# Optimization experiments

Measured on AMD Instinct MI355X. Metric: run time of the kernel, lower is better.

The kernel has to match this reference:

```python
import jax, jax.numpy as jnp
import numpy as np

B, T, C, HD = 8, 2048, 1024, 64  # batch, seq, feature_size, head_dim = C // n_head


def setup_inputs() -> dict:
    key = jax.random.key(0)
    kx, kq, kk, kv = jax.random.split(key, 4)
    return {
        "x": jax.random.normal(kx, (B, T, C), dtype=jnp.float32),
        "Wq": jax.random.normal(kq, (C, HD), dtype=jnp.float32) * 0.02,
        "Wk": jax.random.normal(kk, (C, HD), dtype=jnp.float32) * 0.02,
        "Wv": jax.random.normal(kv, (C, HD), dtype=jnp.float32) * 0.02,
    }


def reference(x, Wq, Wk, Wv):
    # x: [B, T, C]; W*: [C, HD] (Linear(feature_size, feature_size//n_head, bias=False))
    Bsz, Tlen, Cdim = x.shape
    q = x @ Wq  # [B, T, HD]
    k = x @ Wk
    v = x @ Wv
    scores = jnp.einsum("btd,bsd->bts", q, k)  # [B, T, T]
    causal = jnp.tril(jnp.ones((Tlen, Tlen), dtype=bool))
    # faithful to source: masked_fill(-inf) THEN divide by sqrt(C) (full feature size)
    scores = jnp.where(causal, scores, -jnp.inf) / jnp.sqrt(jnp.float32(Cdim))
    att = jax.nn.softmax(scores, axis=-1)  # dropout p=0.0 (eval) -> identity
    return att @ v  # [B, T, HD]
```

## Files before the change

kernel.cpp:

```cpp
#include <hip/hip_runtime.h>


#define BATCH 8
#define SEQ   2048
#define CIN   1024
#define HDIM  64
#define NROW  (BATCH * SEQ)
#define NQT   (NROW / 16)

typedef __attribute__((ext_vector_type(8))) short bf16x8;
typedef __attribute__((ext_vector_type(4))) short u16x4;
typedef __attribute__((ext_vector_type(4))) float f32x4;

__device__ __forceinline__ unsigned short f2bf(float f) {
  unsigned int u = __builtin_bit_cast(unsigned int, f);
  u += 0x7fffu + ((u >> 16) & 1u);
  return (unsigned short)(u >> 16);
}
__device__ __forceinline__ float bf2f(unsigned short h) {
  return __builtin_bit_cast(float, (unsigned int)h << 16);
}
__device__ __forceinline__ u16x4 pack4(f32x4 a) {
  u16x4 r;
  r[0] = (short)f2bf(a[0]); r[1] = (short)f2bf(a[1]);
  r[2] = (short)f2bf(a[2]); r[3] = (short)f2bf(a[3]);
  return r;
}

__global__ __launch_bounds__(256) void wtrans_k(const float* __restrict__ wq,
                                                const float* __restrict__ wk,
                                                const float* __restrict__ wv,
                                                unsigned short* __restrict__ wt) {
  __shared__ unsigned short lds[64][65];
  const int m  = blockIdx.x >> 4;
  const int c0 = (blockIdx.x & 15) * 64;
  const float* w = (m == 0) ? wq : (m == 1) ? wk : wv;
  const int nl = threadIdx.x & 63, gr = threadIdx.x >> 6;
#pragma unroll
  for (int i = 0; i < 16; ++i) {
    int cl = gr * 16 + i;
    lds[cl][nl] = f2bf(w[(size_t)(c0 + cl) * HDIM + nl]);
  }
  __syncthreads();
#pragma unroll
  for (int i = 0; i < 16; ++i) {
    int n = gr * 16 + i;
    wt[(size_t)m * 65536 + n * CIN + c0 + nl] = lds[nl][n];
  }
}

__global__ __launch_bounds__(512) void qkv_proj_k(const float* __restrict__ x,
                                                  const unsigned short* __restrict__ wt,
                                                  unsigned short* __restrict__ q,
                                                  unsigned short* __restrict__ k,
                                                  unsigned short* __restrict__ vt) {
  __shared__ __align__(16) unsigned char ldsb[28672];
  const int tid  = threadIdx.x;
  const int lane = tid & 63;
  const int w    = tid >> 6;
  const int lr   = lane & 15, lg = lane >> 4;
  const int wm   = w & 1, wn = w >> 1;
  const int row0 = blockIdx.x * 32;

  const int trow  = tid >> 4;
  const int tcol4 = (tid & 15) * 4;
  const float* xg = x + (size_t)(row0 + trow) * CIN + tcol4;
  const int xoff  = trow * 128 + (((tcol4 >> 3) ^ (trow & 7)) << 4) + ((tcol4 & 4) << 1);

  const int wrow_ = tid >> 3;
  const int wg8   = tid & 7;
  const unsigned short* wg[3];
  int woff[3];
#pragma unroll
  for (int c = 0; c < 3; ++c) {
    int wrow = c * 64 + wrow_;
    wg[c]   = wt + (size_t)wrow * CIN + wg8 * 8;
    woff[c] = 4096 + wrow * 128 + ((wg8 ^ (wrow & 7)) << 4);
  }

  f32x4 acc[3];
#pragma unroll
  for (int i = 0; i < 3; ++i) acc[i] = (f32x4){0.f, 0.f, 0.f, 0.f};

  const int arow_off = (wm * 16 + lr) * 128;
  const int brow0    = wn * 48 + lr;

#pragma unroll 1
  for (int t = 0; t < 16; ++t) {
    const int k0 = t * 64;
    f32x4 xv = *(const f32x4*)(xg + k0);
    bf16x8 w0 = *(const bf16x8*)(wg[0] + k0);
    bf16x8 w1 = *(const bf16x8*)(wg[1] + k0);
    bf16x8 w2 = *(const bf16x8*)(wg[2] + k0);
    __syncthreads();
    *(u16x4*)(void*)(ldsb + xoff)    = pack4(xv);
    *(bf16x8*)(void*)(ldsb + woff[0]) = w0;
    *(bf16x8*)(void*)(ldsb + woff[1]) = w1;
    *(bf16x8*)(void*)(ldsb + woff[2]) = w2;
    __syncthreads();
#pragma unroll
    for (int kk = 0; kk < 2; ++kk) {
      const int swz = (((kk << 2) | lg) ^ (lr & 7)) << 4;
      bf16x8 af = *(const bf16x8*)(void*)(ldsb + arow_off + swz);
#pragma unroll
      for (int f = 0; f < 3; ++f) {
        bf16x8 bf_ = *(const bf16x8*)(void*)(ldsb + 4096 + (brow0 + f * 16) * 128 + swz);
        acc[f] = __builtin_amdgcn_mfma_f32_16x16x32_bf16(af, bf_, acc[f], 0, 0, 0);
      }
    }
  }

#pragma unroll
  for (int f = 0; f < 3; ++f) {
    const int gc  = wn * 48 + f * 16;
    const int mat = gc >> 6;
    const int hd  = (gc & 63) + lr;
#pragma unroll
    for (int j = 0; j < 4; ++j) {
      int grow = row0 + wm * 16 + lg * 4 + j;
      float v = acc[f][j];
      if (mat == 0) {
        q[(size_t)grow * HDIM + hd] = f2bf(v * 0.03125f);
      } else if (mat == 1) {
        k[(size_t)grow * HDIM + hd] = f2bf(v);
      } else {
        int b = grow >> 11, tp = grow & 2047;
        vt[((size_t)b * HDIM + hd) * SEQ + tp] = f2bf(v);
      }
    }
  }
}

__global__ __launch_bounds__(64) void attn_k(const unsigned short* __restrict__ q,
                                             const unsigned short* __restrict__ k,
                                             const unsigned short* __restrict__ vt,
                                             float* __restrict__ opart,
                                             float* __restrict__ m_l,
                                             int S) {
  __shared__ __align__(16) unsigned short plds[16][72];
  const int lane = threadIdx.x;
  const int lr = lane & 15, lg = lane >> 4;
  const int blk  = blockIdx.x;
  const int b    = blk & 7;
  const int rest = blk >> 3;
  const int s    = rest % S;
  const int qt   = 127 - rest / S;
  const int row0 = qt * 16;
  const int p    = (b * 128 + qt) * S + s;

  const unsigned short* qb_ = q  + (size_t)b * SEQ * HDIM;
  const unsigned short* kb_ = k  + (size_t)b * SEQ * HDIM;
  const unsigned short* vb_ = vt + (size_t)b * HDIM * SEQ;

  bf16x8 qf0 = *(const bf16x8*)(qb_ + (row0 + lr) * HDIM + lg * 8);
  bf16x8 qf1 = *(const bf16x8*)(qb_ + (row0 + lr) * HDIM + 32 + lg * 8);

  f32x4 o[4];
#pragma unroll
  for (int n = 0; n < 4; ++n) o[n] = (f32x4){0.f, 0.f, 0.f, 0.f};
  float m_run = -INFINITY, l_run = 0.f;
  const int   qrow = row0 + lr;
  const float LOG2E = 1.44269504f;
  const int nt = (row0 + 79) >> 6;
  const int lo = (nt * s) / S;
  const int hi = (nt * (s + 1)) / S;

  for (int t = lo; t < hi; ++t) {
    const int kv = t * 64;
    f32x4 sv[4];
#pragma unroll
    for (int f = 0; f < 4; ++f) sv[f] = (f32x4){0.f, 0.f, 0.f, 0.f};
#pragma unroll
    for (int f = 0; f < 4; ++f) {
      bf16x8 ka0 = *(const bf16x8*)(kb_ + (kv + f * 16 + lr) * HDIM + lg * 8);
      bf16x8 ka1 = *(const bf16x8*)(kb_ + (kv + f * 16 + lr) * HDIM + 32 + lg * 8);
      sv[f] = __builtin_amdgcn_mfma_f32_16x16x32_bf16(ka0, qf0, sv[f], 0, 0, 0);
      sv[f] = __builtin_amdgcn_mfma_f32_16x16x32_bf16(ka1, qf1, sv[f], 0, 0, 0);
    }
    if (kv + 63 > row0) {
#pragma unroll
      for (int f = 0; f < 4; ++f)
#pragma unroll
        for (int j = 0; j < 4; ++j)
          if (kv + f * 16 + lg * 4 + j > qrow) sv[f][j] = -INFINITY;
    }
    float tm = -INFINITY;
#pragma unroll
    for (int f = 0; f < 4; ++f)
#pragma unroll
      for (int j = 0; j < 4; ++j) tm = fmaxf(tm, sv[f][j]);
    tm = fmaxf(tm, __shfl_xor(tm, 16, 64));
    tm = fmaxf(tm, __shfl_xor(tm, 32, 64));
    float m_new = fmaxf(m_run, tm);
    float alpha = (m_run == -INFINITY) ? 0.f : exp2f((m_run - m_new) * LOG2E);
    float mc    = (m_new == -INFINITY) ? 0.f : m_new * LOG2E;
    float ps = 0.f;
#pragma unroll
    for (int f = 0; f < 4; ++f) {
      float p0 = exp2f(sv[f][0] * LOG2E - mc);
      float p1 = exp2f(sv[f][1] * LOG2E - mc);
      float p2 = exp2f(sv[f][2] * LOG2E - mc);
      float p3 = exp2f(sv[f][3] * LOG2E - mc);
      unsigned short r0 = f2bf(p0), r1 = f2bf(p1), r2 = f2bf(p2), r3 = f2bf(p3);
      *(unsigned int*)(&plds[lr][f * 16 + lg * 4])     = (unsigned int)r0 | ((unsigned int)r1 << 16);
      *(unsigned int*)(&plds[lr][f * 16 + lg * 4 + 2]) = (unsigned int)r2 | ((unsigned int)r3 << 16);
      ps += bf2f(r0) + bf2f(r1) + bf2f(r2) + bf2f(r3);
    }
    ps += __shfl_xor(ps, 16, 64);
    ps += __shfl_xor(ps, 32, 64);
    l_run = l_run * alpha + ps;
    m_run = m_new;
#pragma unroll
    for (int j = 0; j < 4; ++j) {
      float aj = __shfl(alpha, lg * 4 + j, 64);
      o[0][j] *= aj; o[1][j] *= aj; o[2][j] *= aj; o[3][j] *= aj;
    }
    __syncthreads();
#pragma unroll
    for (int kk = 0; kk < 2; ++kk) {
      bf16x8 pf = *(const bf16x8*)(&plds[lr][kk * 32 + lg * 8]);
#pragma unroll
      for (int n = 0; n < 4; ++n) {
        bf16x8 vf = *(const bf16x8*)(vb_ + (n * 16 + lr) * SEQ + kv + kk * 32 + lg * 8);
        o[n] = __builtin_amdgcn_mfma_f32_16x16x32_bf16(pf, vf, o[n], 0, 0, 0);
      }
    }
    __syncthreads();
  }

  if (lane < 16) {
    m_l[p * 32 + lane]      = m_run;
    m_l[p * 32 + 16 + lane] = l_run;
  }
#pragma unroll
  for (int j = 0; j < 4; ++j) {
    int r = lg * 4 + j;
#pragma unroll
    for (int n = 0; n < 4; ++n)
      opart[(size_t)p * 1024 + r * 64 + n * 16 + lr] = o[n][j];
  }
}

__global__ __launch_bounds__(256) void combine_k(const float* __restrict__ opart,
                                                 const float* __restrict__ m_l,
                                                 float* __restrict__ out, int S) {
  const float LOG2E = 1.44269504f;
  int idx = blockIdx.x * 256 + threadIdx.x;
  int col = idx & 63;
  int row = idx >> 6;
  int b = row >> 11, t = row & 2047;
  int qt = t >> 4, r = t & 15;
  int pb = (b * 128 + qt) * S;
  float M = -INFINITY;
  for (int s = 0; s < S; ++s) M = fmaxf(M, m_l[(pb + s) * 32 + r]);
  float l = 0.f, o = 0.f;
  for (int s = 0; s < S; ++s) {
    float ms = m_l[(pb + s) * 32 + r];
    float w  = exp2f((ms - M) * LOG2E);
    l += m_l[(pb + s) * 32 + 16 + r] * w;
    o += opart[(size_t)(pb + s) * 1024 + r * 64 + col] * w;
  }
  out[(size_t)row * HDIM + col] = o / l;
}

extern "C" void kernel_launch(void* const* d_in, const int* in_sizes, int n_in,
                              void* d_out, int out_size, void* d_ws, size_t ws_size,
                              hipStream_t stream) {
  const float* x  = (const float*)d_in[0];
  const float* wq = (const float*)d_in[1];
  const float* wk = (const float*)d_in[2];
  const float* wv = (const float*)d_in[3];
  float* outp = (float*)d_out;

  const size_t bf_bytes = ((size_t)3 * NROW * HDIM + 3 * 65536) * 2;
  int S = 4;
  while (S > 1 && (size_t)NQT * S * (32 + 1024) * 4 + bf_bytes > ws_size) S >>= 1;

  float* m_l   = (float*)d_ws;
  float* opart = m_l + (size_t)NQT * S * 32;
  unsigned short* qbuf = (unsigned short*)(opart + (size_t)NQT * S * 1024);
  unsigned short* kbuf = qbuf + (size_t)NROW * HDIM;
  unsigned short* vbuf = kbuf + (size_t)NROW * HDIM;
  unsigned short* wt   = vbuf + (size_t)NROW * HDIM;

  hipLaunchKernelGGL(wtrans_k, dim3(48), dim3(256), 0, stream, wq, wk, wv, wt);
  hipLaunchKernelGGL(qkv_proj_k, dim3(NROW / 32), dim3(512), 0, stream, x, wt, qbuf, kbuf, vbuf);
  hipLaunchKernelGGL(attn_k, dim3(NQT * S), dim3(64), 0, stream, qbuf, kbuf, vbuf, opart, m_l, S);
  hipLaunchKernelGGL(combine_k, dim3(NROW * HDIM / 256), dim3(256), 0, stream, opart, m_l, outp, S);
}
```

Before: 162.6 us.

## Pack four attention waves per block, prefetch K/V tiles, drop block barriers

The attention kernel now runs four independent 64-lane work units per 256-thread block, each with its own shared-memory P buffer. Block-wide __syncthreads are replaced by an LDS waitcnt plus a scheduling barrier. The next K tile is prefetched into registers while the current one is processed, and V fragments are loaded before the softmax so their latency overlaps the exp work. The row sum now uses the fp32 probabilities instead of the bf16-rounded ones. These changes raise register pressure and may lower occupancy.

```diff
diff --git a/kernel.cpp b/kernel.cpp
--- a/kernel.cpp
+++ b/kernel.cpp
@@ -131,22 +131,24 @@
   }
 }
 
-__global__ __launch_bounds__(64) void attn_k(const unsigned short* __restrict__ q,
-                                             const unsigned short* __restrict__ k,
-                                             const unsigned short* __restrict__ vt,
-                                             float* __restrict__ opart,
-                                             float* __restrict__ m_l,
-                                             int S) {
-  __shared__ __align__(16) unsigned short plds[16][72];
-  const int lane = threadIdx.x;
+__global__ __launch_bounds__(256) void attn_k(const unsigned short* __restrict__ q,
+                                              const unsigned short* __restrict__ k,
+                                              const unsigned short* __restrict__ vt,
+                                              float* __restrict__ opart,
+                                              float* __restrict__ m_l,
+                                              int S) {
+  __shared__ __align__(16) unsigned short plds[4][16][72];
+  const int lane = threadIdx.x & 63;
+  const int w    = threadIdx.x >> 6;
   const int lr = lane & 15, lg = lane >> 4;
-  const int blk  = blockIdx.x;
-  const int b    = blk & 7;
-  const int rest = blk >> 3;
+  const int u    = blockIdx.x * 4 + w;
+  const int b    = u & 7;
+  const int rest = u >> 3;
   const int s    = rest % S;
   const int qt   = 127 - rest / S;
   const int row0 = qt * 16;
   const int p    = (b * 128 + qt) * S + s;
+  unsigned short (*pw)[72] = plds[w];
 
   const unsigned short* qb_ = q  + (size_t)b * SEQ * HDIM;
   const unsigned short* kb_ = k  + (size_t)b * SEQ * HDIM;
@@ -165,18 +167,36 @@
   const int lo = (nt * s) / S;
   const int hi = (nt * (s + 1)) / S;
 
+  auto LDK = [&](int kv, bf16x8* dst) {
+#pragma unroll
+    for (int f = 0; f < 4; ++f) {
+      dst[2 * f]     = *(const bf16x8*)(kb_ + (kv + f * 16 + lr) * HDIM + lg * 8);
+      dst[2 * f + 1] = *(const bf16x8*)(kb_ + (kv + f * 16 + lr) * HDIM + 32 + lg * 8);
+    }
+  };
+
+  bf16x8 ka[8];
+  if (lo < hi) LDK(lo * 64, ka);
+
   for (int t = lo; t < hi; ++t) {
     const int kv = t * 64;
     f32x4 sv[4];
 #pragma unroll
-    for (int f = 0; f < 4; ++f) sv[f] = (f32x4){0.f, 0.f, 0.f, 0.f};
-#pragma unroll
     for (int f = 0; f < 4; ++f) {
-      bf16x8 ka0 = *(const bf16x8*)(kb_ + (kv + f * 16 + lr) * HDIM + lg * 8);
-      bf16x8 ka1 = *(const bf16x8*)(kb_ + (kv + f * 16 + lr) * HDIM + 32 + lg * 8);
-      sv[f] = __builtin_amdgcn_mfma_f32_16x16x32_bf16(ka0, qf0, sv[f], 0, 0, 0);
-      sv[f] = __builtin_amdgcn_mfma_f32_16x16x32_bf16(ka1, qf1, sv[f], 0, 0, 0);
-    }
+      sv[f] = (f32x4){0.f, 0.f, 0.f, 0.f};
+      sv[f] = __builtin_amdgcn_mfma_f32_16x16x32_bf16(ka[2 * f],     qf0, sv[f], 0, 0, 0);
+      sv[f] = __builtin_amdgcn_mfma_f32_16x16x32_bf16(ka[2 * f + 1], qf1, sv[f], 0, 0, 0);
+    }
+    bf16x8 kn[8];
+    const bool more = (t + 1 < hi);
+    if (more) LDK(kv + 64, kn);
+    bf16x8 vf[8];
+#pragma unroll
+    for (int kk = 0; kk < 2; ++kk)
+#pragma unroll
+      for (int n = 0; n < 4; ++n)
+        vf[kk * 4 + n] = *(const bf16x8*)(vb_ + (n * 16 + lr) * SEQ + kv + kk * 32 + lg * 8);
+
     if (kv + 63 > row0) {
 #pragma unroll
       for (int f = 0; f < 4; ++f)
@@ -201,10 +221,11 @@
       float p1 = exp2f(sv[f][1] * LOG2E - mc);
       float p2 = exp2f(sv[f][2] * LOG2E - mc);
       float p3 = exp2f(sv[f][3] * LOG2E - mc);
-      unsigned short r0 = f2bf(p0), r1 = f2bf(p1), r2 = f2bf(p2), r3 = f2bf(p3);
-      *(unsigned int*)(&plds[lr][f * 16 + lg * 4])     = (unsigned int)r0 | ((unsigned int)r1 << 16);
-      *(unsigned int*)(&plds[lr][f * 16 + lg * 4 + 2]) = (unsigned int)r2 | ((unsigned int)r3 << 16);
-      ps += bf2f(r0) + bf2f(r1) + bf2f(r2) + bf2f(r3);
+      ps += (p0 + p1) + (p2 + p3);
+      unsigned int lo32 = (unsigned int)f2bf(p0) | ((unsigned int)f2bf(p1) << 16);
+      unsigned int hi32 = (unsigned int)f2bf(p2) | ((unsigned int)f2bf(p3) << 16);
+      uint2 pk; pk.x = lo32; pk.y = hi32;
+      *(uint2*)(&pw[lr][f * 16 + lg * 4]) = pk;
     }
     ps += __shfl_xor(ps, 16, 64);
     ps += __shfl_xor(ps, 32, 64);
@@ -215,17 +236,19 @@
       float aj = __shfl(alpha, lg * 4 + j, 64);
       o[0][j] *= aj; o[1][j] *= aj; o[2][j] *= aj; o[3][j] *= aj;
     }
-    __syncthreads();
+    asm volatile("s_waitcnt lgkmcnt(0)" ::: "memory");
+    __builtin_amdgcn_sched_barrier(0);
 #pragma unroll
     for (int kk = 0; kk < 2; ++kk) {
-      bf16x8 pf = *(const bf16x8*)(&plds[lr][kk * 32 + lg * 8]);
-#pragma unroll
-      for (int n = 0; n < 4; ++n) {
-        bf16x8 vf = *(const bf16x8*)(vb_ + (n * 16 + lr) * SEQ + kv + kk * 32 + lg * 8);
-        o[n] = __builtin_amdgcn_mfma_f32_16x16x32_bf16(pf, vf, o[n], 0, 0, 0);
-      }
-    }
-    __syncthreads();
+      bf16x8 pf = *(const bf16x8*)(&pw[lr][kk * 32 + lg * 8]);
+#pragma unroll
+      for (int n = 0; n < 4; ++n)
+        o[n] = __builtin_amdgcn_mfma_f32_16x16x32_bf16(pf, vf[kk * 4 + n], o[n], 0, 0, 0);
+    }
+    if (more) {
+#pragma unroll
+      for (int f = 0; f < 8; ++f) ka[f] = kn[f];
+    }
   }
 
   if (lane < 16) {
@@ -285,6 +308,6 @@
 
   hipLaunchKernelGGL(wtrans_k, dim3(48), dim3(256), 0, stream, wq, wk, wv, wt);
   hipLaunchKernelGGL(qkv_proj_k, dim3(NROW / 32), dim3(512), 0, stream, x, wt, qbuf, kbuf, vbuf);
-  hipLaunchKernelGGL(attn_k, dim3(NQT * S), dim3(64), 0, stream, qbuf, kbuf, vbuf, opart, m_l, S);
+  hipLaunchKernelGGL(attn_k, dim3(NQT * S / 4), dim3(256), 0, stream, qbuf, kbuf, vbuf, opart, m_l, S);
   hipLaunchKernelGGL(combine_k, dim3(NROW * HDIM / 256), dim3(256), 0, stream, opart, m_l, outp, S);
 }
```

After: 162.2 us. Within noise of the previous version (-0.3%).

## Balance causal attention with split count growing by query tile, pack four waves per block

Applied to the files above, without the earlier changes.

Replaces the fixed per-tile KV split with a variable split count that grows with query-tile index (S = qt/16 + 1), so each work unit covers a roughly equal number of KV tiles. Four independent wavefronts now share one 256-thread block, each with its own LDS slice, and the block-wide barriers become an LDS waitcnt plus a sched barrier. Row sums now come from the fp32 probabilities rather than the bf16-rounded ones, and the combine kernel decodes the new unit layout. It aims to remove tail imbalance and barrier cost, in exchange for extra index arithmetic and a workspace size that no longer adapts to ws_size.

```diff
diff --git a/kernel.cpp b/kernel.cpp
--- a/kernel.cpp
+++ b/kernel.cpp
@@ -7,6 +7,7 @@
 #define HDIM  64
 #define NROW  (BATCH * SEQ)
 #define NQT   (NROW / 16)
+#define UNITS 576
 
 typedef __attribute__((ext_vector_type(8))) short bf16x8;
 typedef __attribute__((ext_vector_type(4))) short u16x4;
@@ -131,22 +132,28 @@
   }
 }
 
-__global__ __launch_bounds__(64) void attn_k(const unsigned short* __restrict__ q,
-                                             const unsigned short* __restrict__ k,
-                                             const unsigned short* __restrict__ vt,
-                                             float* __restrict__ opart,
-                                             float* __restrict__ m_l,
-                                             int S) {
-  __shared__ __align__(16) unsigned short plds[16][72];
-  const int lane = threadIdx.x;
+__global__ __launch_bounds__(256) void attn_k(const unsigned short* __restrict__ q,
+                                              const unsigned short* __restrict__ k,
+                                              const unsigned short* __restrict__ vt,
+                                              float* __restrict__ opart,
+                                              float* __restrict__ m_l) {
+  __shared__ __align__(16) unsigned short plds[4][16][72];
+  const int lane = threadIdx.x & 63;
+  const int w    = threadIdx.x >> 6;
   const int lr = lane & 15, lg = lane >> 4;
-  const int blk  = blockIdx.x;
-  const int b    = blk & 7;
-  const int rest = blk >> 3;
-  const int s    = rest % S;
-  const int qt   = 127 - rest / S;
+  const int u    = blockIdx.x * 4 + w;
+  const int b    = u / UNITS;
+  const int unit = u - b * UNITS;
+  int a = 0;
+#pragma unroll
+  for (int i = 0; i < 7; ++i) if (8 * (a + 1) * (a + 2) <= unit) ++a;
+  const int S    = a + 1;
+  const int rem  = unit - 8 * a * S;
+  const int qt   = 16 * a + rem / S;
+  const int seg  = rem - (rem / S) * S;
   const int row0 = qt * 16;
-  const int p    = (b * 128 + qt) * S + s;
+  const int p    = b * UNITS + unit;
+  unsigned short (*pw)[72] = plds[w];
 
   const unsigned short* qb_ = q  + (size_t)b * SEQ * HDIM;
   const unsigned short* kb_ = k  + (size_t)b * SEQ * HDIM;
@@ -161,19 +168,18 @@
   float m_run = -INFINITY, l_run = 0.f;
   const int   qrow = row0 + lr;
   const float LOG2E = 1.44269504f;
-  const int nt = (row0 + 79) >> 6;
-  const int lo = (nt * s) / S;
-  const int hi = (nt * (s + 1)) / S;
+  const int nt = (qt >> 2) + 1;
+  const int lo = (nt * seg) / S;
+  const int hi = (nt * (seg + 1)) / S;
 
   for (int t = lo; t < hi; ++t) {
     const int kv = t * 64;
     f32x4 sv[4];
 #pragma unroll
-    for (int f = 0; f < 4; ++f) sv[f] = (f32x4){0.f, 0.f, 0.f, 0.f};
-#pragma unroll
     for (int f = 0; f < 4; ++f) {
       bf16x8 ka0 = *(const bf16x8*)(kb_ + (kv + f * 16 + lr) * HDIM + lg * 8);
       bf16x8 ka1 = *(const bf16x8*)(kb_ + (kv + f * 16 + lr) * HDIM + 32 + lg * 8);
+      sv[f] = (f32x4){0.f, 0.f, 0.f, 0.f};
       sv[f] = __builtin_amdgcn_mfma_f32_16x16x32_bf16(ka0, qf0, sv[f], 0, 0, 0);
       sv[f] = __builtin_amdgcn_mfma_f32_16x16x32_bf16(ka1, qf1, sv[f], 0, 0, 0);
     }
@@ -201,10 +207,11 @@
       float p1 = exp2f(sv[f][1] * LOG2E - mc);
       float p2 = exp2f(sv[f][2] * LOG2E - mc);
       float p3 = exp2f(sv[f][3] * LOG2E - mc);
-      unsigned short r0 = f2bf(p0), r1 = f2bf(p1), r2 = f2bf(p2), r3 = f2bf(p3);
-      *(unsigned int*)(&plds[lr][f * 16 + lg * 4])     = (unsigned int)r0 | ((unsigned int)r1 << 16);
-      *(unsigned int*)(&plds[lr][f * 16 + lg * 4 + 2]) = (unsigned int)r2 | ((unsigned int)r3 << 16);
-      ps += bf2f(r0) + bf2f(r1) + bf2f(r2) + bf2f(r3);
+      ps += (p0 + p1) + (p2 + p3);
+      unsigned int lo32 = (unsigned int)f2bf(p0) | ((unsigned int)f2bf(p1) << 16);
+      unsigned int hi32 = (unsigned int)f2bf(p2) | ((unsigned int)f2bf(p3) << 16);
+      uint2 pk; pk.x = lo32; pk.y = hi32;
+      *(uint2*)(&pw[lr][f * 16 + lg * 4]) = pk;
     }
     ps += __shfl_xor(ps, 16, 64);
     ps += __shfl_xor(ps, 32, 64);
@@ -215,17 +222,17 @@
       float aj = __shfl(alpha, lg * 4 + j, 64);
       o[0][j] *= aj; o[1][j] *= aj; o[2][j] *= aj; o[3][j] *= aj;
     }
-    __syncthreads();
+    asm volatile("s_waitcnt lgkmcnt(0)" ::: "memory");
+    __builtin_amdgcn_sched_barrier(0);
 #pragma unroll
     for (int kk = 0; kk < 2; ++kk) {
-      bf16x8 pf = *(const bf16x8*)(&plds[lr][kk * 32 + lg * 8]);
+      bf16x8 pf = *(const bf16x8*)(&pw[lr][kk * 32 + lg * 8]);
 #pragma unroll
       for (int n = 0; n < 4; ++n) {
         bf16x8 vf = *(const bf16x8*)(vb_ + (n * 16 + lr) * SEQ + kv + kk * 32 + lg * 8);
         o[n] = __builtin_amdgcn_mfma_f32_16x16x32_bf16(pf, vf, o[n], 0, 0, 0);
       }
     }
-    __syncthreads();
   }
 
   if (lane < 16) {
@@ -243,14 +250,16 @@
 
 __global__ __launch_bounds__(256) void combine_k(const float* __restrict__ opart,
                                                  const float* __restrict__ m_l,
-                                                 float* __restrict__ out, int S) {
+                                                 float* __restrict__ out) {
   const float LOG2E = 1.44269504f;
   int idx = blockIdx.x * 256 + threadIdx.x;
   int col = idx & 63;
   int row = idx >> 6;
   int b = row >> 11, t = row & 2047;
   int qt = t >> 4, r = t & 15;
-  int pb = (b * 128 + qt) * S;
+  int a = qt >> 4;
+  int S = a + 1;
+  int pb = b * UNITS + 8 * a * S + (qt & 15) * S;
   float M = -INFINITY;
   for (int s = 0; s < S; ++s) M = fmaxf(M, m_l[(pb + s) * 32 + r]);
   float l = 0.f, o = 0.f;
@@ -272,19 +281,16 @@
   const float* wv = (const float*)d_in[3];
   float* outp = (float*)d_out;
 
-  const size_t bf_bytes = ((size_t)3 * NROW * HDIM + 3 * 65536) * 2;
-  int S = 4;
-  while (S > 1 && (size_t)NQT * S * (32 + 1024) * 4 + bf_bytes > ws_size) S >>= 1;
-
+  const int NP = BATCH * UNITS;
   float* m_l   = (float*)d_ws;
-  float* opart = m_l + (size_t)NQT * S * 32;
-  unsigned short* qbuf = (unsigned short*)(opart + (size_t)NQT * S * 1024);
+  float* opart = m_l + (size_t)NP * 32;
+  unsigned short* qbuf = (unsigned short*)(opart + (size_t)NP * 1024);
   unsigned short* kbuf = qbuf + (size_t)NROW * HDIM;
   unsigned short* vbuf = kbuf + (size_t)NROW * HDIM;
   unsigned short* wt   = vbuf + (size_t)NROW * HDIM;
 
   hipLaunchKernelGGL(wtrans_k, dim3(48), dim3(256), 0, stream, wq, wk, wv, wt);
   hipLaunchKernelGGL(qkv_proj_k, dim3(NROW / 32), dim3(512), 0, stream, x, wt, qbuf, kbuf, vbuf);
-  hipLaunchKernelGGL(attn_k, dim3(NQT * S), dim3(64), 0, stream, qbuf, kbuf, vbuf, opart, m_l, S);
-  hipLaunchKernelGGL(combine_k, dim3(NROW * HDIM / 256), dim3(256), 0, stream, opart, m_l, outp, S);
-}
+  hipLaunchKernelGGL(attn_k, dim3(NP / 4), dim3(256), 0, stream, qbuf, kbuf, vbuf, opart, m_l);
+  hipLaunchKernelGGL(combine_k, dim3(NROW * HDIM / 256), dim3(256), 0, stream, opart, m_l, outp);
+}
```

Result: slower. 169.2 us (+4.0%).
